# Kernel tuning notes

Hardware: AMD Instinct MI355X
Metric: run time of the kernel (lower is better)

Reference implementation:

```python
import jax, jax.numpy as jnp
import numpy as np

B, T, D = 4, 2048, 2048
DV = 1024
T_IMG, N_LAT = 8, 64
H, DH = 16, 64
INNER = H * DH
EPS = 1e-5


def setup_inputs() -> dict:
    key = jax.random.key(0)
    ks = jax.random.split(key, 8)
    x = jax.random.normal(ks[0], (B, T, D), dtype=jnp.float32)
    media = jax.random.normal(ks[1], (B, T_IMG, N_LAT, DV), dtype=jnp.float32)
    # exactly T_IMG media tokens per sequence, evenly spaced
    pos = (jnp.arange(T_IMG) + 1) * (T // (T_IMG + 1))
    media_locations = jnp.zeros((B, T), dtype=bool).at[:, pos].set(True)
    gamma = jnp.ones((D,), dtype=jnp.float32)
    beta = jnp.zeros((D,), dtype=jnp.float32)
    Wq = jax.random.normal(ks[2], (D, INNER), dtype=jnp.float32) * (D ** -0.5)
    Wkv = jax.random.normal(ks[3], (DV, 2 * INNER), dtype=jnp.float32) * (DV ** -0.5)
    Wout = jax.random.normal(ks[4], (INNER, D), dtype=jnp.float32) * (INNER ** -0.5)
    return {"x": x, "media": media, "media_locations": media_locations,
            "gamma": gamma, "beta": beta, "Wq": Wq, "Wkv": Wkv, "Wout": Wout}


def reference(x, media, media_locations, gamma, beta, Wq, Wkv, Wout):
    scale = DH ** -0.5
    # LayerNorm
    mu = jnp.mean(x, axis=-1, keepdims=True)
    var = jnp.mean(jnp.square(x - mu), axis=-1, keepdims=True)
    xn = (x - mu) * jax.lax.rsqrt(var + EPS) * gamma + beta
    q = xn @ Wq                                   # (B,T,INNER)
    media_f = media.reshape(B, T_IMG * N_LAT, DV)  # (B,J,DV)
    kv = media_f @ Wkv                             # (B,J,2*INNER)
    k, v = jnp.split(kv, 2, axis=-1)
    q = q.reshape(B, T, H, DH).transpose(0, 2, 1, 3) * scale   # (B,H,T,DH)
    k = k.reshape(B, -1, H, DH).transpose(0, 2, 1, 3)          # (B,H,J,DH)
    v = v.reshape(B, -1, H, DH).transpose(0, 2, 1, 3)
    sim = jnp.einsum('bhid,bhjd->bhij', q, k)      # (B,H,T,J)
    # media-location mask: text attends only to its immediately preceding media
    text_time = jnp.cumsum(media_locations.astype(jnp.int32), axis=-1)  # (B,T)
    media_time = jnp.arange(T_IMG, dtype=jnp.int32) + 1                 # (J_img,)
    media_time = jnp.repeat(media_time, N_LAT)                          # (J,)
    mask = text_time[:, None, :, None] == media_time[None, None, None, :]  # (B,1,T,J)
    neg = -jnp.finfo(sim.dtype).max
    sim = jnp.where(mask, sim, neg)
    sim = sim - jax.lax.stop_gradient(jnp.max(sim, axis=-1, keepdims=True))
    attn = jax.nn.softmax(sim, axis=-1)
    # zero attention for text positions with no preceding media
    no_media = (text_time == 0)[:, None, :, None]  # (B,1,T,1)
    attn = jnp.where(no_media, 0.0, attn)
    out = jnp.einsum('bhij,bhjd->bhid', attn, v)   # (B,H,T,DH)
    out = out.transpose(0, 2, 1, 3).reshape(B, T, INNER)
    return out @ Wout
```

## Files before the change

kernel.cpp:

```cpp
#include <hip/hip_runtime.h>
#include <hip/hip_bf16.h>

#define B_ 4
#define T_ 2048
#define D_ 2048
#define DV_ 1024
#define TIMG_ 8
#define NLAT_ 64
#define H_ 16
#define DH_ 64
#define INNER_ 1024
#define J_ (TIMG_ * NLAT_)

using f32x4 = __attribute__((ext_vector_type(4))) float;
using bf16x8 = __attribute__((ext_vector_type(8))) short;
using bf16x4 = __attribute__((ext_vector_type(4))) short;

__device__ __forceinline__ unsigned short f2bf(float f) {
  union { float f; unsigned int u; } c{f};
  unsigned int r = c.u + 0x7FFFu + ((c.u >> 16) & 1u);
  return (unsigned short)(r >> 16);
}

__device__ __forceinline__ void stage16(const unsigned short* g, unsigned short* l) {
  __builtin_amdgcn_global_load_lds(
      (const __attribute__((address_space(1))) unsigned int*)g,
      (__attribute__((address_space(3))) unsigned int*)l, 16, 0, 0);
}

__global__ __launch_bounds__(256) void prep_kernel(
    const float* __restrict__ x, const void* __restrict__ locs,
    const float* __restrict__ g, const float* __restrict__ bta,
    const float* __restrict__ Wq, const float* __restrict__ Wkv,
    const float* __restrict__ Wout, const float* __restrict__ media,
    unsigned short* __restrict__ xn, int* __restrict__ img_idx,
    unsigned short* __restrict__ wqt, unsigned short* __restrict__ wkvt,
    unsigned short* __restrict__ woutt, unsigned short* __restrict__ medb) {
  __shared__ __align__(16) float smf[64 * 68];
  const int tid = threadIdx.x;
  int blk = blockIdx.x;

  if (blk < 2048) {
    const int lane = tid & 63;
    const int row = blk * 4 + (tid >> 6);
    const float4* xr = (const float4*)(x + (size_t)row * D_);
    float4 v[8];
#pragma unroll
    for (int i = 0; i < 8; ++i) v[i] = xr[i * 64 + lane];
    float s = 0.f, sq = 0.f;
#pragma unroll
    for (int i = 0; i < 8; ++i) {
      s += v[i].x + v[i].y + v[i].z + v[i].w;
      sq += v[i].x * v[i].x + v[i].y * v[i].y + v[i].z * v[i].z + v[i].w * v[i].w;
    }
#pragma unroll
    for (int off = 32; off > 0; off >>= 1) {
      s += __shfl_xor(s, off);
      sq += __shfl_xor(sq, off);
    }
    const float mu = s * (1.0f / D_);
    const float rstd = rsqrtf(sq * (1.0f / D_) - mu * mu + 1e-5f);
    const float4* gv4 = (const float4*)g;
    const float4* bv4 = (const float4*)bta;
    ushort4* o4 = (ushort4*)(xn + (size_t)row * D_);
#pragma unroll
    for (int i = 0; i < 8; ++i) {
      float4 gv = gv4[i * 64 + lane];
      float4 bv = bv4[i * 64 + lane];
      o4[i * 64 + lane] = make_ushort4(f2bf((v[i].x - mu) * rstd * gv.x + bv.x),
                                       f2bf((v[i].y - mu) * rstd * gv.y + bv.y),
                                       f2bf((v[i].z - mu) * rstd * gv.z + bv.z),
                                       f2bf((v[i].w - mu) * rstd * gv.w + bv.w));
    }
    return;
  }
  blk -= 2048;
  if (blk < 4) {
    int* sm = (int*)smf;
    const int b = blk;
    const unsigned char* u8 = (const unsigned char*)locs;
    int cnt = 0;
    for (int i = tid; i < B_ * T_; i += 256) cnt += (u8[i] != 0) ? 1 : 0;
    sm[tid] = cnt;
    __syncthreads();
    for (int off = 128; off > 0; off >>= 1) {
      if (tid < off) sm[tid] += sm[tid + off];
      __syncthreads();
    }
    const bool u8mode = (sm[0] == B_ * TIMG_);
    __syncthreads();
    const int base = b * T_ + tid * 8;
    const int* i32 = (const int*)locs;
    int v[8];
    int ts = 0;
#pragma unroll
    for (int j = 0; j < 8; ++j) {
      v[j] = u8mode ? (u8[base + j] != 0 ? 1 : 0) : (i32[base + j] != 0 ? 1 : 0);
      ts += v[j];
    }
    sm[tid] = ts;
    __syncthreads();
    for (int off = 1; off < 256; off <<= 1) {
      int add = (tid >= off) ? sm[tid - off] : 0;
      __syncthreads();
      sm[tid] += add;
      __syncthreads();
    }
    int acc = sm[tid] - ts;
#pragma unroll
    for (int j = 0; j < 8; ++j) {
      acc += v[j];
      img_idx[base + j] = acc - 1;
    }
    return;
  }
  blk -= 4;
  if (blk < 1536) {
    const float* tin;
    unsigned short* tout;
    int R, C, bx, by;
    float scale = 1.0f;
    if (blk < 512) {
      tin = Wq; tout = wqt; R = D_; C = INNER_; by = blk >> 4; bx = blk & 15; scale = 0.125f;
    } else if (blk < 1024) {
      blk -= 512;
      tin = Wkv; tout = wkvt; R = DV_; C = 2 * INNER_; by = blk >> 5; bx = blk & 31;
    } else {
      blk -= 1024;
      tin = Wout; tout = woutt; R = INNER_; C = D_; by = blk >> 5; bx = blk & 31;
    }
    const int br = by * 64, bc = bx * 64;
    float (*tile)[68] = (float(*)[68])smf;
    const int r = tid >> 4;
    const int c4 = (tid & 15) * 4;
#pragma unroll
    for (int rr = 0; rr < 4; ++rr)
      *(float4*)&tile[r + rr * 16][c4] =
          *(const float4*)&tin[(size_t)(br + r + rr * 16) * C + bc + c4];
    __syncthreads();
    const int oc = tid >> 2;
    const int rb = (tid & 3) * 16;
    bf16x8 o0, o1;
#pragma unroll
    for (int e = 0; e < 8; ++e) {
      o0[e] = (short)f2bf(tile[rb + e][oc] * scale);
      o1[e] = (short)f2bf(tile[rb + 8 + e][oc] * scale);
    }
    unsigned short* op = tout + (size_t)(bc + oc) * R + br + rb;
    *(bf16x8*)op = o0;
    *(bf16x8*)(op + 8) = o1;
    return;
  }
  blk -= 1536;
  const int i = blk * 512 + tid * 2;
  float4 a = ((const float4*)media)[i];
  float4 b2 = ((const float4*)media)[i + 1];
  ((ushort4*)medb)[i] = make_ushort4(f2bf(a.x), f2bf(a.y), f2bf(a.z), f2bf(a.w));
  ((ushort4*)medb)[i + 1] = make_ushort4(f2bf(b2.x), f2bf(b2.y), f2bf(b2.z), f2bf(b2.w));
}

__global__ void vtrans(const unsigned short* __restrict__ kvb, unsigned short* __restrict__ vt) {
  __shared__ unsigned short tile[32][33];
  const int jt = blockIdx.x * 32;
  const int dt = blockIdx.y * 32;
  const int b = blockIdx.z;
  const int tx = threadIdx.x, ty = threadIdx.y;
#pragma unroll
  for (int i = ty; i < 32; i += 8)
    tile[i][tx] = kvb[(size_t)(b * J_ + jt + i) * (2 * INNER_) + INNER_ + dt + tx];
  __syncthreads();
#pragma unroll
  for (int i = ty; i < 32; i += 8)
    vt[(size_t)(b * INNER_ + dt + i) * J_ + jt + tx] = tile[tx][i];
}

template <bool BF16OUT>
__global__ __launch_bounds__(512, 2) void gemm_bt2(const unsigned short* __restrict__ Ag,
                                                   const unsigned short* __restrict__ Bg,
                                                   void* __restrict__ Cv,
                                                   int M, int N, int K) {
  __shared__ __align__(16) unsigned short lds[65536];
  const int tid = threadIdx.x;
  const int lane = tid & 63;
  const int wave = tid >> 6;
  const int l15 = lane & 15;
  const int lg8 = (lane >> 4) << 3;
  const int wr64 = (wave >> 2) << 6;
  const int wc16 = (wave & 3) << 4;

  const int nwg = gridDim.x;
  int wg = ((int)blockIdx.x & 7) * (nwg >> 3) + ((int)blockIdx.x >> 3);
  const int gridM = M >> 7;
  const long row0 = (long)(wg % gridM) << 7;
  const long col0 = (long)(wg / gridM) << 8;

  auto stA = [&](int t, int r) {
    const int i = r * 512 + tid;
    const int row = i >> 3;
    const int c = (i & 7) ^ (row & 7);
    stage16(Ag + (size_t)(row0 + row) * K + (t << 6) + c * 8,
            &lds[(t & 1) * 8192 + i * 8]);
  };
  auto stB = [&](int t, int r) {
    const int i = r * 512 + tid;
    const int row = i >> 3;
    const int c = (i & 7) ^ (row & 7);
    stage16(Bg + (size_t)(col0 + row) * K + (t << 6) + c * 8,
            &lds[16384 + (t % 3) * 16384 + i * 8]);
  };

  const int NT = K >> 6;
  stB(0, 0); stB(0, 1); stB(0, 2); stB(0, 3);
  stA(0, 0); stA(0, 1);
  stB(1, 0); stB(1, 1); stB(1, 2); stB(1, 3);
  asm volatile("s_waitcnt vmcnt(4)" ::: "memory");
  asm volatile("s_barrier" ::: "memory");

  f32x4 acc[4][4] = {};
  for (int t = 0; t < NT; ++t) {
    const unsigned short* Ab = &lds[(t & 1) * 8192];
    const unsigned short* Bb = &lds[16384 + (t % 3) * 16384];
    bf16x8 af[4][2], bfr[4][2];
#pragma unroll
    for (int m = 0; m < 4; ++m)
#pragma unroll
      for (int kk = 0; kk < 2; ++kk) {
        const int row = wr64 + m * 16 + l15;
        af[m][kk] = *(const bf16x8*)(Ab + row * 64 + ((kk * 32 + lg8) ^ ((row & 7) << 3)));
      }
#pragma unroll
    for (int n = 0; n < 2; ++n)
#pragma unroll
      for (int kk = 0; kk < 2; ++kk) {
        const int brow = n * 64 + wc16 + l15;
        bfr[n][kk] = *(const bf16x8*)(Bb + brow * 64 + ((kk * 32 + lg8) ^ ((brow & 7) << 3)));
      }
    if (t + 1 < NT) { stA(t + 1, 0); stA(t + 1, 1); }
    if (t + 2 < NT) { stB(t + 2, 0); stB(t + 2, 1); }
    asm volatile("s_barrier" ::: "memory");
    asm volatile("s_waitcnt lgkmcnt(0)" ::: "memory");
    __builtin_amdgcn_s_setprio(1);
#pragma unroll
    for (int m = 0; m < 4; ++m)
#pragma unroll
      for (int n = 0; n < 2; ++n)
#pragma unroll
        for (int kk = 0; kk < 2; ++kk)
          acc[m][n] = __builtin_amdgcn_mfma_f32_16x16x32_bf16(af[m][kk], bfr[n][kk], acc[m][n], 0, 0, 0);
    __builtin_amdgcn_s_setprio(0);
    asm volatile("s_barrier" ::: "memory");
#pragma unroll
    for (int n = 2; n < 4; ++n)
#pragma unroll
      for (int kk = 0; kk < 2; ++kk) {
        const int brow = n * 64 + wc16 + l15;
        bfr[n][kk] = *(const bf16x8*)(Bb + brow * 64 + ((kk * 32 + lg8) ^ ((brow & 7) << 3)));
      }
    if (t + 2 < NT) {
      stB(t + 2, 2); stB(t + 2, 3);
      asm volatile("s_waitcnt vmcnt(4)" ::: "memory");
    } else {
      asm volatile("s_waitcnt vmcnt(0)" ::: "memory");
    }
    asm volatile("s_barrier" ::: "memory");
    asm volatile("s_waitcnt lgkmcnt(0)" ::: "memory");
    __builtin_amdgcn_s_setprio(1);
#pragma unroll
    for (int m = 0; m < 4; ++m)
#pragma unroll
      for (int n = 2; n < 4; ++n)
#pragma unroll
        for (int kk = 0; kk < 2; ++kk)
          acc[m][n] = __builtin_amdgcn_mfma_f32_16x16x32_bf16(af[m][kk], bfr[n][kk], acc[m][n], 0, 0, 0);
    __builtin_amdgcn_s_setprio(0);
    asm volatile("s_barrier" ::: "memory");
  }

  const int cr = (lane >> 4) << 2;
#pragma unroll
  for (int m = 0; m < 4; ++m)
#pragma unroll
    for (int n = 0; n < 4; ++n)
#pragma unroll
      for (int j = 0; j < 4; ++j) {
        const size_t idx = (row0 + wr64 + m * 16 + cr + j) * (size_t)N + col0 + n * 64 + wc16 + l15;
        if constexpr (BF16OUT)
          ((unsigned short*)Cv)[idx] = f2bf(acc[m][n][j]);
        else
          ((float*)Cv)[idx] = acc[m][n][j];
      }
}

template <bool BF16OUT>
__global__ __launch_bounds__(512, 2) void gemm256(const unsigned short* __restrict__ Ag,
                                                  const unsigned short* __restrict__ Bg,
                                                  void* __restrict__ Cv,
                                                  int M, int N, int K) {
  __shared__ __align__(16) unsigned short lds[2][32768];
  const int tid = threadIdx.x;
  const int lane = tid & 63;
  const int wave = tid >> 6;
  const int l15 = lane & 15;
  const int lg8 = (lane >> 4) << 3;
  const int wm = (wave >> 2) << 7;
  const int wn = (wave & 3) << 6;

  const int nwg = gridDim.x;
  int wg = ((int)blockIdx.x & 7) * (nwg >> 3) + ((int)blockIdx.x >> 3);
  const int gridM = M >> 8;
  const long row0 = (long)(wg % gridM) << 8;
  const long col0 = (long)(wg / gridM) << 8;

  auto stA = [&](int buf, int kt, int r) {
    const int i = r * 512 + tid;
    const int row = i >> 3;
    const int c = (i & 7) ^ (row & 7);
    stage16(Ag + (size_t)(row0 + row) * K + kt + c * 8, &lds[buf][i * 8]);
  };
  auto stB = [&](int buf, int kt, int r) {
    const int i = r * 512 + tid;
    const int row = i >> 3;
    const int c = (i & 7) ^ (row & 7);
    stage16(Bg + (size_t)(col0 + row) * K + kt + c * 8, &lds[buf][16384 + i * 8]);
  };

  const int NT = K >> 6;
  stB(0, 0, 0); stB(0, 0, 1); stB(0, 0, 2); stB(0, 0, 3);
  stA(0, 0, 0); stA(0, 0, 1); stA(0, 0, 2); stA(0, 0, 3);
  stB(1, 64, 0); stB(1, 64, 1); stB(1, 64, 2); stB(1, 64, 3);
  asm volatile("s_waitcnt vmcnt(4)" ::: "memory");
  asm volatile("s_barrier" ::: "memory");

  f32x4 acc[8][4] = {};
  int cur = 0;
  for (int t = 0; t < NT; ++t, cur ^= 1) {
    const unsigned short* Ab = &lds[cur][0];
    const unsigned short* Bb = &lds[cur][16384];
    bf16x8 af[4][2], bfr[4][2];
    const int ktn = (t + 1) << 6;
    const int ktn2 = (t + 2) << 6;
#pragma unroll
    for (int m = 0; m < 4; ++m)
#pragma unroll
      for (int kk = 0; kk < 2; ++kk) {
        const int row = wm + m * 16 + l15;
        af[m][kk] = *(const bf16x8*)(Ab + row * 64 + ((kk * 32 + lg8) ^ ((row & 7) << 3)));
      }
#pragma unroll
    for (int n = 0; n < 2; ++n)
#pragma unroll
      for (int kk = 0; kk < 2; ++kk) {
        const int brow = wn + n * 16 + l15;
        bfr[n][kk] = *(const bf16x8*)(Bb + brow * 64 + ((kk * 32 + lg8) ^ ((brow & 7) << 3)));
      }
    if (t + 1 < NT) { stA(cur ^ 1, ktn, 0); stA(cur ^ 1, ktn, 1); }
    asm volatile("s_barrier" ::: "memory");
    asm volatile("s_waitcnt lgkmcnt(0)" ::: "memory");
    __builtin_amdgcn_s_setprio(1);
#pragma unroll
    for (int m = 0; m < 4; ++m)
#pragma unroll
      for (int n = 0; n < 2; ++n)
#pragma unroll
        for (int kk = 0; kk < 2; ++kk)
          acc[m][n] = __builtin_amdgcn_mfma_f32_16x16x32_bf16(af[m][kk], bfr[n][kk], acc[m][n], 0, 0, 0);
    __builtin_amdgcn_s_setprio(0);
    asm volatile("s_barrier" ::: "memory");
#pragma unroll
    for (int n = 2; n < 4; ++n)
#pragma unroll
      for (int kk = 0; kk < 2; ++kk) {
        const int brow = wn + n * 16 + l15;
        bfr[n][kk] = *(const bf16x8*)(Bb + brow * 64 + ((kk * 32 + lg8) ^ ((brow & 7) << 3)));
      }
    if (t + 1 < NT) { stA(cur ^ 1, ktn, 2); stA(cur ^ 1, ktn, 3); }
    asm volatile("s_barrier" ::: "memory");
    asm volatile("s_waitcnt lgkmcnt(0)" ::: "memory");
    __builtin_amdgcn_s_setprio(1);
#pragma unroll
    for (int m = 0; m < 4; ++m)
#pragma unroll
      for (int n = 2; n < 4; ++n)
#pragma unroll
        for (int kk = 0; kk < 2; ++kk)
          acc[m][n] = __builtin_amdgcn_mfma_f32_16x16x32_bf16(af[m][kk], bfr[n][kk], acc[m][n], 0, 0, 0);
    __builtin_amdgcn_s_setprio(0);
    asm volatile("s_barrier" ::: "memory");
#pragma unroll
    for (int m = 0; m < 4; ++m)
#pragma unroll
      for (int kk = 0; kk < 2; ++kk) {
        const int row = wm + (m + 4) * 16 + l15;
        af[m][kk] = *(const bf16x8*)(Ab + row * 64 + ((kk * 32 + lg8) ^ ((row & 7) << 3)));
      }
    if (t + 2 < NT) { stB(cur, ktn2, 0); stB(cur, ktn2, 1); }
    asm volatile("s_barrier" ::: "memory");
    asm volatile("s_waitcnt lgkmcnt(0)" ::: "memory");
    __builtin_amdgcn_s_setprio(1);
#pragma unroll
    for (int m = 0; m < 4; ++m)
#pragma unroll
      for (int n = 0; n < 2; ++n)
#pragma unroll
        for (int kk = 0; kk < 2; ++kk)
          acc[m + 4][n] = __builtin_amdgcn_mfma_f32_16x16x32_bf16(af[m][kk], bfr[n][kk], acc[m + 4][n], 0, 0, 0);
    __builtin_amdgcn_s_setprio(0);
    asm volatile("s_barrier" ::: "memory");
    if (t + 2 < NT) { stB(cur, ktn2, 2); stB(cur, ktn2, 3); }
    asm volatile("s_waitcnt vmcnt(4)" ::: "memory");
    asm volatile("s_barrier" ::: "memory");
    __builtin_amdgcn_s_setprio(1);
#pragma unroll
    for (int m = 0; m < 4; ++m)
#pragma unroll
      for (int n = 2; n < 4; ++n)
#pragma unroll
        for (int kk = 0; kk < 2; ++kk)
          acc[m + 4][n] = __builtin_amdgcn_mfma_f32_16x16x32_bf16(af[m][kk], bfr[n][kk], acc[m + 4][n], 0, 0, 0);
    __builtin_amdgcn_s_setprio(0);
    asm volatile("s_barrier" ::: "memory");
  }

  const int cr = (lane >> 4) << 2;
#pragma unroll
  for (int m = 0; m < 8; ++m)
#pragma unroll
    for (int n = 0; n < 4; ++n)
#pragma unroll
      for (int j = 0; j < 4; ++j) {
        const size_t idx = (row0 + wm + m * 16 + cr + j) * (size_t)N + col0 + wn + n * 16 + l15;
        if constexpr (BF16OUT)
          ((unsigned short*)Cv)[idx] = f2bf(acc[m][n][j]);
        else
          ((float*)Cv)[idx] = acc[m][n][j];
      }
}

__global__ __launch_bounds__(256) void attn2_kernel(
    const unsigned short* __restrict__ qb,
    const unsigned short* __restrict__ kvb,
    const unsigned short* __restrict__ vt,
    const int* __restrict__ img_idx,
    unsigned short* __restrict__ attn_out) {
  __shared__ unsigned short Pl[4][64 * 72];
  const int tid = threadIdx.x;
  const int lane = tid & 63;
  const int w = tid >> 6;
  int bid = blockIdx.x;
  const int hg = bid & 3; bid >>= 2;
  const int tile = bid & 31; bid >>= 5;
  const int b = bid;
  const int t0 = tile * 64;
  const int h = hg * 4 + w;
  const int l15 = lane & 15;
  const int lg = lane >> 4;

  const int* ii = img_idx + b * T_ + t0;
  int myimg = ii[lane];
  int tmin = myimg, tmax = myimg;
#pragma unroll
  for (int off = 1; off < 64; off <<= 1) {
    tmin = min(tmin, __shfl_xor(tmin, off));
    tmax = max(tmax, __shfl_xor(tmax, off));
  }
  unsigned short* op = attn_out + (size_t)(b * T_ + t0) * INNER_ + h * DH_;
  if (tmin < 0) {
    for (int r = 0; r < 64; ++r)
      if (ii[r] < 0) op[(size_t)r * INNER_ + lane] = 0;
  }
  if (tmax < 0) return;

  bf16x8 qa[4][2];
  const unsigned short* qrow = qb + (size_t)(b * T_ + t0) * INNER_ + h * DH_;
#pragma unroll
  for (int m = 0; m < 4; ++m)
#pragma unroll
    for (int kk = 0; kk < 2; ++kk)
      qa[m][kk] = *(const bf16x8*)(qrow + (size_t)(l15 + m * 16) * INNER_ + kk * 32 + lg * 8);

  unsigned short* pw = Pl[w];
  for (int img = max(tmin, 0); img <= tmax; ++img) {
    const unsigned short* Kb = kvb + (size_t)(b * J_ + img * NLAT_) * (2 * INNER_) + h * DH_;
    f32x4 acc[4][4] = {};
#pragma unroll
    for (int kk = 0; kk < 2; ++kk) {
      bf16x8 bfr[4];
#pragma unroll
      for (int n = 0; n < 4; ++n)
        bfr[n] = *(const bf16x8*)(Kb + (size_t)(l15 + n * 16) * (2 * INNER_) + kk * 32 + lg * 8);
#pragma unroll
      for (int m = 0; m < 4; ++m)
#pragma unroll
        for (int n = 0; n < 4; ++n)
          acc[m][n] = __builtin_amdgcn_mfma_f32_16x16x32_bf16(qa[m][kk], bfr[n], acc[m][n], 0, 0, 0);
    }
#pragma unroll
    for (int m = 0; m < 4; ++m) {
#pragma unroll
      for (int j = 0; j < 4; ++j) {
        float mx = fmaxf(fmaxf(acc[m][0][j], acc[m][1][j]), fmaxf(acc[m][2][j], acc[m][3][j]));
#pragma unroll
        for (int off = 1; off < 16; off <<= 1) mx = fmaxf(mx, __shfl_xor(mx, off));
        float sum = 0.f;
#pragma unroll
        for (int n = 0; n < 4; ++n) {
          float e = __expf(acc[m][n][j] - mx);
          acc[m][n][j] = e;
          sum += e;
        }
#pragma unroll
        for (int off = 1; off < 16; off <<= 1) sum += __shfl_xor(sum, off);
        const float ri = 1.0f / sum;
        const int row = m * 16 + lg * 4 + j;
#pragma unroll
        for (int n = 0; n < 4; ++n)
          pw[row * 72 + n * 16 + l15] = f2bf(acc[m][n][j] * ri);
      }
    }
    const unsigned short* Vb = vt + (size_t)(b * INNER_ + h * DH_) * J_ + img * NLAT_;
    f32x4 oacc[4][4] = {};
#pragma unroll
    for (int kk = 0; kk < 2; ++kk) {
      bf16x8 pa[4], bfr[4];
#pragma unroll
      for (int m = 0; m < 4; ++m) {
        bf16x4 lo = *(const bf16x4*)(pw + (m * 16 + l15) * 72 + kk * 32 + lg * 8);
        bf16x4 hi = *(const bf16x4*)(pw + (m * 16 + l15) * 72 + kk * 32 + lg * 8 + 4);
        bf16x8 v;
#pragma unroll
        for (int e = 0; e < 4; ++e) { v[e] = lo[e]; v[e + 4] = hi[e]; }
        pa[m] = v;
      }
#pragma unroll
      for (int n = 0; n < 4; ++n)
        bfr[n] = *(const bf16x8*)(Vb + (size_t)(l15 + n * 16) * J_ + kk * 32 + lg * 8);
#pragma unroll
      for (int m = 0; m < 4; ++m)
#pragma unroll
        for (int n = 0; n < 4; ++n)
          oacc[m][n] = __builtin_amdgcn_mfma_f32_16x16x32_bf16(pa[m], bfr[n], oacc[m][n], 0, 0, 0);
    }
#pragma unroll
    for (int m = 0; m < 4; ++m)
#pragma unroll
      for (int j = 0; j < 4; ++j) {
        const int row = m * 16 + lg * 4 + j;
        if (ii[row] == img) {
#pragma unroll
          for (int n = 0; n < 4; ++n)
            op[(size_t)row * INNER_ + n * 16 + l15] = f2bf(oacc[m][n][j]);
        }
      }
  }
}

extern "C" void kernel_launch(void* const* d_in, const int* in_sizes, int n_in,
                              void* d_out, int out_size, void* d_ws, size_t ws_size,
                              hipStream_t stream) {
  const float* x = (const float*)d_in[0];
  const float* media = (const float*)d_in[1];
  const void* mloc = d_in[2];
  const float* gamma = (const float*)d_in[3];
  const float* beta = (const float*)d_in[4];
  const float* Wq = (const float*)d_in[5];
  const float* Wkv = (const float*)d_in[6];
  const float* Wout = (const float*)d_in[7];
  float* out = (float*)d_out;

  char* ws = (char*)d_ws;
  unsigned short* xn = (unsigned short*)(ws);
  unsigned short* wqt = (unsigned short*)(ws + 33554432);
  unsigned short* wkvt = (unsigned short*)(ws + 37748736);
  unsigned short* woutt = (unsigned short*)(ws + 41943040);
  unsigned short* medb = (unsigned short*)(ws + 46137344);
  unsigned short* qb = (unsigned short*)(ws + 50331648);
  unsigned short* kvb = (unsigned short*)(ws + 67108864);
  unsigned short* vt = (unsigned short*)(ws + 75497472);
  int* img_idx = (int*)(ws + 79691776);
  unsigned short* attn_out = xn;

  prep_kernel<<<4612, 256, 0, stream>>>(x, mloc, gamma, beta, Wq, Wkv, Wout, media,
                                        xn, img_idx, wqt, wkvt, woutt, medb);
  gemm_bt2<true><<<(B_ * T_ / 128) * (INNER_ / 256), 512, 0, stream>>>(xn, wqt, qb, B_ * T_, INNER_, D_);
  gemm_bt2<true><<<(B_ * J_ / 128) * (2 * INNER_ / 256), 512, 0, stream>>>(medb, wkvt, kvb, B_ * J_, 2 * INNER_, DV_);
  vtrans<<<dim3(J_ / 32, INNER_ / 32, B_), dim3(32, 8), 0, stream>>>(kvb, vt);
  attn2_kernel<<<B_ * (T_ / 64) * 4, 256, 0, stream>>>(qb, kvb, vt, img_idx, attn_out);
  gemm256<false><<<(B_ * T_ / 256) * (D_ / 256), 512, 0, stream>>>(attn_out, woutt, out, B_ * T_, D_, INNER_);
}
```

Measured before the change: 156.7 us.

## Split prep kernel and fuse remaining prep work into the Q-projection GEMM launch

```diff
diff --git a/kernel.cpp b/kernel.cpp
--- a/kernel.cpp
+++ b/kernel.cpp
@@ -28,14 +28,10 @@
       (__attribute__((address_space(3))) unsigned int*)l, 16, 0, 0);
 }
 
-__global__ __launch_bounds__(256) void prep_kernel(
-    const float* __restrict__ x, const void* __restrict__ locs,
-    const float* __restrict__ g, const float* __restrict__ bta,
-    const float* __restrict__ Wq, const float* __restrict__ Wkv,
-    const float* __restrict__ Wout, const float* __restrict__ media,
-    unsigned short* __restrict__ xn, int* __restrict__ img_idx,
-    unsigned short* __restrict__ wqt, unsigned short* __restrict__ wkvt,
-    unsigned short* __restrict__ woutt, unsigned short* __restrict__ medb) {
+__global__ __launch_bounds__(256) void prepA_kernel(
+    const float* __restrict__ x, const float* __restrict__ g,
+    const float* __restrict__ bta, const float* __restrict__ Wq,
+    unsigned short* __restrict__ xn, unsigned short* __restrict__ wqt) {
   __shared__ __align__(16) float smf[64 * 68];
   const int tid = threadIdx.x;
   int blk = blockIdx.x;
@@ -75,9 +71,138 @@
     return;
   }
   blk -= 2048;
-  if (blk < 4) {
-    int* sm = (int*)smf;
-    const int b = blk;
+  const int by = blk >> 4, bx = blk & 15;
+  const int br = by * 64, bc = bx * 64;
+  float (*tile)[68] = (float(*)[68])smf;
+  const int r = tid >> 4;
+  const int c4 = (tid & 15) * 4;
+#pragma unroll
+  for (int rr = 0; rr < 4; ++rr)
+    *(float4*)&tile[r + rr * 16][c4] =
+        *(const float4*)&Wq[(size_t)(br + r + rr * 16) * INNER_ + bc + c4];
+  __syncthreads();
+  const int oc = tid >> 2;
+  const int rb = (tid & 3) * 16;
+  bf16x8 o0, o1;
+#pragma unroll
+  for (int e = 0; e < 8; ++e) {
+    o0[e] = (short)f2bf(tile[rb + e][oc] * 0.125f);
+    o1[e] = (short)f2bf(tile[rb + 8 + e][oc] * 0.125f);
+  }
+  unsigned short* op = wqt + (size_t)(bc + oc) * D_ + br + rb;
+  *(bf16x8*)op = o0;
+  *(bf16x8*)(op + 8) = o1;
+}
+
+template <bool BF16OUT>
+__device__ __forceinline__ void gemm128_body(int wg, unsigned char* smem,
+                                             const unsigned short* Ag,
+                                             const unsigned short* Bg,
+                                             void* Cv, int M, int N, int K) {
+  unsigned short* lds = (unsigned short*)smem;
+  const int tid = threadIdx.x;
+  const int lane = tid & 63;
+  const int wave = tid >> 6;
+  const int l15 = lane & 15;
+  const int kg = lane >> 4;
+  const int wm = (wave >> 1) << 6;
+  const int wn = (wave & 1) << 6;
+  const int gridM = M >> 7;
+  const long row0 = (long)(wg % gridM) << 7;
+  const long col0 = (long)(wg / gridM) << 7;
+
+  auto stT = [&](const unsigned short* G, long base0, int t, int r, int bufoff) {
+    const int j = r * 256 + tid;
+    const int rp = j >> 3;
+    const int u = (j & 7) ^ (rp & 7);
+    const int row = (rp << 1) | (u >> 2);
+    const int k8 = (u & 3) << 3;
+    stage16(G + (base0 + row) * K + (t << 5) + k8, &lds[bufoff + j * 8]);
+  };
+
+  const int NT = K >> 5;
+  stT(Bg, col0, 0, 0, 8192); stT(Bg, col0, 0, 1, 8192);
+  stT(Ag, row0, 0, 0, 0);    stT(Ag, row0, 0, 1, 0);
+  stT(Bg, col0, 1, 0, 8192 + 4096); stT(Bg, col0, 1, 1, 8192 + 4096);
+  asm volatile("s_waitcnt vmcnt(2)" ::: "memory");
+  asm volatile("s_barrier" ::: "memory");
+
+  f32x4 acc[4][4] = {};
+  for (int t = 0; t < NT; ++t) {
+    const unsigned short* Ab = &lds[(t & 1) * 4096];
+    const unsigned short* Bb = &lds[8192 + (t % 3) * 4096];
+    bf16x8 af[4], bfr[4];
+#pragma unroll
+    for (int m = 0; m < 4; ++m) {
+      const int r = wm + m * 16 + l15;
+      const int rp = r >> 1;
+      const int s = (((r & 1) << 2) | kg) ^ (rp & 7);
+      af[m] = *(const bf16x8*)(Ab + rp * 64 + s * 8);
+    }
+#pragma unroll
+    for (int n = 0; n < 4; ++n) {
+      const int r = wn + n * 16 + l15;
+      const int rp = r >> 1;
+      const int s = (((r & 1) << 2) | kg) ^ (rp & 7);
+      bfr[n] = *(const bf16x8*)(Bb + rp * 64 + s * 8);
+    }
+    if (t + 1 < NT) {
+      stT(Ag, row0, t + 1, 0, ((t + 1) & 1) * 4096);
+      stT(Ag, row0, t + 1, 1, ((t + 1) & 1) * 4096);
+    }
+    if (t + 2 < NT) {
+      stT(Bg, col0, t + 2, 0, 8192 + ((t + 2) % 3) * 4096);
+      stT(Bg, col0, t + 2, 1, 8192 + ((t + 2) % 3) * 4096);
+    }
+    asm volatile("s_waitcnt lgkmcnt(0)" ::: "memory");
+    __builtin_amdgcn_s_setprio(1);
+#pragma unroll
+    for (int m = 0; m < 4; ++m)
+#pragma unroll
+      for (int n = 0; n < 4; ++n)
+        acc[m][n] = __builtin_amdgcn_mfma_f32_16x16x32_bf16(af[m], bfr[n], acc[m][n], 0, 0, 0);
+    __builtin_amdgcn_s_setprio(0);
+    if (t + 2 < NT)
+      asm volatile("s_waitcnt vmcnt(2)" ::: "memory");
+    else
+      asm volatile("s_waitcnt vmcnt(0)" ::: "memory");
+    asm volatile("s_barrier" ::: "memory");
+  }
+
+  const int cr = (lane >> 4) << 2;
+#pragma unroll
+  for (int m = 0; m < 4; ++m)
+#pragma unroll
+    for (int n = 0; n < 4; ++n)
+#pragma unroll
+      for (int j = 0; j < 4; ++j) {
+        const size_t idx = (row0 + wm + m * 16 + cr + j) * (size_t)N + col0 + wn + n * 16 + l15;
+        if constexpr (BF16OUT)
+          ((unsigned short*)Cv)[idx] = f2bf(acc[m][n][j]);
+        else
+          ((float*)Cv)[idx] = acc[m][n][j];
+      }
+}
+
+__global__ __launch_bounds__(256, 4) void g1_fused(
+    const unsigned short* __restrict__ xn, const unsigned short* __restrict__ wqt,
+    unsigned short* __restrict__ qb,
+    const void* __restrict__ locs, const float* __restrict__ Wkv,
+    const float* __restrict__ Wout, const float* __restrict__ media,
+    int* __restrict__ img_idx, unsigned short* __restrict__ wkvt,
+    unsigned short* __restrict__ woutt, unsigned short* __restrict__ medb) {
+  __shared__ __align__(16) unsigned char smem[40960];
+  const int tid = threadIdx.x;
+  const int bid = blockIdx.x;
+  const bool isg = (bid < 2560) && (bid % 5 == 0);
+  if (isg) {
+    gemm128_body<true>(bid / 5, smem, xn, wqt, qb, B_ * T_, INNER_, D_);
+    return;
+  }
+  int pid = (bid < 2560) ? bid - bid / 5 - 1 : bid - 512;
+  if (pid < 4) {
+    int* sm = (int*)smem;
+    const int b = pid;
     const unsigned char* u8 = (const unsigned char*)locs;
     int cnt = 0;
     for (int i = tid; i < B_ * T_; i += 256) cnt += (u8[i] != 0) ? 1 : 0;
@@ -114,45 +239,36 @@
     }
     return;
   }
-  blk -= 4;
-  if (blk < 1536) {
-    const float* tin;
-    unsigned short* tout;
-    int R, C, bx, by;
-    float scale = 1.0f;
-    if (blk < 512) {
-      tin = Wq; tout = wqt; R = D_; C = INNER_; by = blk >> 4; bx = blk & 15; scale = 0.125f;
-    } else if (blk < 1024) {
-      blk -= 512;
-      tin = Wkv; tout = wkvt; R = DV_; C = 2 * INNER_; by = blk >> 5; bx = blk & 31;
-    } else {
-      blk -= 1024;
-      tin = Wout; tout = woutt; R = INNER_; C = D_; by = blk >> 5; bx = blk & 31;
-    }
+  pid -= 4;
+  if (pid < 1024) {
+    const float* tin = (pid < 512) ? Wkv : Wout;
+    unsigned short* tout = (pid < 512) ? wkvt : woutt;
+    int blk = pid & 511;
+    const int by = blk >> 5, bx = blk & 31;
     const int br = by * 64, bc = bx * 64;
-    float (*tile)[68] = (float(*)[68])smf;
+    float (*tile)[68] = (float(*)[68])smem;
     const int r = tid >> 4;
     const int c4 = (tid & 15) * 4;
 #pragma unroll
     for (int rr = 0; rr < 4; ++rr)
       *(float4*)&tile[r + rr * 16][c4] =
-          *(const float4*)&tin[(size_t)(br + r + rr * 16) * C + bc + c4];
+          *(const float4*)&tin[(size_t)(br + r + rr * 16) * (2 * INNER_) + bc + c4];
     __syncthreads();
     const int oc = tid >> 2;
     const int rb = (tid & 3) * 16;
     bf16x8 o0, o1;
 #pragma unroll
     for (int e = 0; e < 8; ++e) {
-      o0[e] = (short)f2bf(tile[rb + e][oc] * scale);
-      o1[e] = (short)f2bf(tile[rb + 8 + e][oc] * scale);
-    }
-    unsigned short* op = tout + (size_t)(bc + oc) * R + br + rb;
+      o0[e] = (short)f2bf(tile[rb + e][oc]);
+      o1[e] = (short)f2bf(tile[rb + 8 + e][oc]);
+    }
+    unsigned short* op = tout + (size_t)(bc + oc) * DV_ + br + rb;
     *(bf16x8*)op = o0;
     *(bf16x8*)(op + 8) = o1;
     return;
   }
-  blk -= 1536;
-  const int i = blk * 512 + tid * 2;
+  pid -= 1024;
+  const int i = pid * 512 + tid * 2;
   float4 a = ((const float4*)media)[i];
   float4 b2 = ((const float4*)media)[i + 1];
   ((ushort4*)medb)[i] = make_ushort4(f2bf(a.x), f2bf(a.y), f2bf(a.z), f2bf(a.w));
@@ -579,9 +695,9 @@
   int* img_idx = (int*)(ws + 79691776);
   unsigned short* attn_out = xn;
 
-  prep_kernel<<<4612, 256, 0, stream>>>(x, mloc, gamma, beta, Wq, Wkv, Wout, media,
-                                        xn, img_idx, wqt, wkvt, woutt, medb);
-  gemm_bt2<true><<<(B_ * T_ / 128) * (INNER_ / 256), 512, 0, stream>>>(xn, wqt, qb, B_ * T_, INNER_, D_);
+  prepA_kernel<<<2560, 256, 0, stream>>>(x, gamma, beta, Wq, xn, wqt);
+  g1_fused<<<2564, 256, 0, stream>>>(xn, wqt, qb, mloc, Wkv, Wout, media,
+                                     img_idx, wkvt, woutt, medb);
   gemm_bt2<true><<<(B_ * J_ / 128) * (2 * INNER_ / 256), 512, 0, stream>>>(medb, wkvt, kvb, B_ * J_, 2 * INNER_, DV_);
   vtrans<<<dim3(J_ / 32, INNER_ / 32, B_), dim3(32, 8), 0, stream>>>(kvb, vt);
   attn2_kernel<<<B_ * (T_ / 64) * 4, 256, 0, stream>>>(qb, kvb, vt, img_idx, attn_out);
```

Result: slower. 178.0 us (+13.6%).

## Fold LayerNorm into Q projection GEMM via gamma-scaled weights and epilogue correction

Applied to the files above, without the earlier changes.

```diff
diff --git a/kernel.cpp b/kernel.cpp
--- a/kernel.cpp
+++ b/kernel.cpp
@@ -29,52 +29,38 @@
 }
 
 __global__ __launch_bounds__(256) void prep_kernel(
-    const float* __restrict__ x, const void* __restrict__ locs,
+    const void* __restrict__ locs,
     const float* __restrict__ g, const float* __restrict__ bta,
     const float* __restrict__ Wq, const float* __restrict__ Wkv,
     const float* __restrict__ Wout, const float* __restrict__ media,
-    unsigned short* __restrict__ xn, int* __restrict__ img_idx,
+    int* __restrict__ img_idx,
     unsigned short* __restrict__ wqt, unsigned short* __restrict__ wkvt,
-    unsigned short* __restrict__ woutt, unsigned short* __restrict__ medb) {
+    unsigned short* __restrict__ woutt, unsigned short* __restrict__ medb,
+    float* __restrict__ uvec, float* __restrict__ vvec) {
   __shared__ __align__(16) float smf[64 * 68];
   const int tid = threadIdx.x;
   int blk = blockIdx.x;
 
-  if (blk < 2048) {
-    const int lane = tid & 63;
-    const int row = blk * 4 + (tid >> 6);
-    const float4* xr = (const float4*)(x + (size_t)row * D_);
-    float4 v[8];
-#pragma unroll
-    for (int i = 0; i < 8; ++i) v[i] = xr[i * 64 + lane];
-    float s = 0.f, sq = 0.f;
-#pragma unroll
-    for (int i = 0; i < 8; ++i) {
-      s += v[i].x + v[i].y + v[i].z + v[i].w;
-      sq += v[i].x * v[i].x + v[i].y * v[i].y + v[i].z * v[i].z + v[i].w * v[i].w;
-    }
-#pragma unroll
-    for (int off = 32; off > 0; off >>= 1) {
-      s += __shfl_xor(s, off);
-      sq += __shfl_xor(sq, off);
-    }
-    const float mu = s * (1.0f / D_);
-    const float rstd = rsqrtf(sq * (1.0f / D_) - mu * mu + 1e-5f);
-    const float4* gv4 = (const float4*)g;
-    const float4* bv4 = (const float4*)bta;
-    ushort4* o4 = (ushort4*)(xn + (size_t)row * D_);
-#pragma unroll
-    for (int i = 0; i < 8; ++i) {
-      float4 gv = gv4[i * 64 + lane];
-      float4 bv = bv4[i * 64 + lane];
-      o4[i * 64 + lane] = make_ushort4(f2bf((v[i].x - mu) * rstd * gv.x + bv.x),
-                                       f2bf((v[i].y - mu) * rstd * gv.y + bv.y),
-                                       f2bf((v[i].z - mu) * rstd * gv.z + bv.z),
-                                       f2bf((v[i].w - mu) * rstd * gv.w + bv.w));
+  if (blk < 16) {
+    const int col = blk * 64 + (tid & 63);
+    const int kc = tid >> 6;
+    float su = 0.f, sv = 0.f;
+    for (int k = kc * 512; k < kc * 512 + 512; ++k) {
+      const float w = Wq[(size_t)k * INNER_ + col];
+      su += g[k] * w;
+      sv += bta[k] * w;
+    }
+    float* s1 = smf;
+    float* s2 = smf + 256;
+    s1[tid] = su; s2[tid] = sv;
+    __syncthreads();
+    if (tid < 64) {
+      uvec[blk * 64 + tid] = 0.125f * (s1[tid] + s1[tid + 64] + s1[tid + 128] + s1[tid + 192]);
+      vvec[blk * 64 + tid] = 0.125f * (s2[tid] + s2[tid + 64] + s2[tid + 128] + s2[tid + 192]);
     }
     return;
   }
-  blk -= 2048;
+  blk -= 16;
   if (blk < 4) {
     int* sm = (int*)smf;
     const int b = blk;
@@ -115,20 +101,8 @@
     return;
   }
   blk -= 4;
-  if (blk < 1536) {
-    const float* tin;
-    unsigned short* tout;
-    int R, C, bx, by;
-    float scale = 1.0f;
-    if (blk < 512) {
-      tin = Wq; tout = wqt; R = D_; C = INNER_; by = blk >> 4; bx = blk & 15; scale = 0.125f;
-    } else if (blk < 1024) {
-      blk -= 512;
-      tin = Wkv; tout = wkvt; R = DV_; C = 2 * INNER_; by = blk >> 5; bx = blk & 31;
-    } else {
-      blk -= 1024;
-      tin = Wout; tout = woutt; R = INNER_; C = D_; by = blk >> 5; bx = blk & 31;
-    }
+  if (blk < 512) {
+    const int by = blk >> 4, bx = blk & 15;
     const int br = by * 64, bc = bx * 64;
     float (*tile)[68] = (float(*)[68])smf;
     const int r = tid >> 4;
@@ -136,27 +110,190 @@
 #pragma unroll
     for (int rr = 0; rr < 4; ++rr)
       *(float4*)&tile[r + rr * 16][c4] =
-          *(const float4*)&tin[(size_t)(br + r + rr * 16) * C + bc + c4];
+          *(const float4*)&Wq[(size_t)(br + r + rr * 16) * INNER_ + bc + c4];
     __syncthreads();
     const int oc = tid >> 2;
     const int rb = (tid & 3) * 16;
     bf16x8 o0, o1;
 #pragma unroll
     for (int e = 0; e < 8; ++e) {
-      o0[e] = (short)f2bf(tile[rb + e][oc] * scale);
-      o1[e] = (short)f2bf(tile[rb + 8 + e][oc] * scale);
-    }
-    unsigned short* op = tout + (size_t)(bc + oc) * R + br + rb;
+      o0[e] = (short)f2bf(tile[rb + e][oc] * g[br + rb + e] * 0.125f);
+      o1[e] = (short)f2bf(tile[rb + 8 + e][oc] * g[br + rb + 8 + e] * 0.125f);
+    }
+    unsigned short* op = wqt + (size_t)(bc + oc) * D_ + br + rb;
     *(bf16x8*)op = o0;
     *(bf16x8*)(op + 8) = o1;
     return;
   }
-  blk -= 1536;
+  blk -= 512;
+  if (blk < 1024) {
+    const float* tin = (blk < 512) ? Wkv : Wout;
+    unsigned short* tout = (blk < 512) ? wkvt : woutt;
+    int idx = blk & 511;
+    const int by = idx >> 5, bx = idx & 31;
+    const int br = by * 64, bc = bx * 64;
+    float (*tile)[68] = (float(*)[68])smf;
+    const int r = tid >> 4;
+    const int c4 = (tid & 15) * 4;
+#pragma unroll
+    for (int rr = 0; rr < 4; ++rr)
+      *(float4*)&tile[r + rr * 16][c4] =
+          *(const float4*)&tin[(size_t)(br + r + rr * 16) * (2 * INNER_) + bc + c4];
+    __syncthreads();
+    const int oc = tid >> 2;
+    const int rb = (tid & 3) * 16;
+    bf16x8 o0, o1;
+#pragma unroll
+    for (int e = 0; e < 8; ++e) {
+      o0[e] = (short)f2bf(tile[rb + e][oc]);
+      o1[e] = (short)f2bf(tile[rb + 8 + e][oc]);
+    }
+    unsigned short* op = tout + (size_t)(bc + oc) * DV_ + br + rb;
+    *(bf16x8*)op = o0;
+    *(bf16x8*)(op + 8) = o1;
+    return;
+  }
+  blk -= 1024;
   const int i = blk * 512 + tid * 2;
   float4 a = ((const float4*)media)[i];
   float4 b2 = ((const float4*)media)[i + 1];
   ((ushort4*)medb)[i] = make_ushort4(f2bf(a.x), f2bf(a.y), f2bf(a.z), f2bf(a.w));
   ((ushort4*)medb)[i + 1] = make_ushort4(f2bf(b2.x), f2bf(b2.y), f2bf(b2.z), f2bf(b2.w));
+}
+
+__global__ __launch_bounds__(512, 2) void gemm1_ln(
+    const float* __restrict__ Xg, const unsigned short* __restrict__ Bg,
+    unsigned short* __restrict__ Cv,
+    const float* __restrict__ uvec, const float* __restrict__ vvec) {
+  const int M = B_ * T_, N = INNER_, K = D_;
+  __shared__ __align__(16) unsigned short lds[65536];
+  const int tid = threadIdx.x;
+  const int lane = tid & 63;
+  const int wave = tid >> 6;
+  const int l15 = lane & 15;
+  const int lg8 = (lane >> 4) << 3;
+  const int wr64 = (wave >> 2) << 6;
+  const int wc16 = (wave & 3) << 4;
+
+  const int nwg = gridDim.x;
+  int wg = ((int)blockIdx.x & 7) * (nwg >> 3) + ((int)blockIdx.x >> 3);
+  const int gridM = M >> 7;
+  const long row0 = (long)(wg % gridM) << 7;
+  const long col0 = (long)(wg / gridM) << 8;
+
+  const int ar = tid >> 2;
+  const int aq = tid & 3;
+  const float4* xrow = (const float4*)(Xg + (size_t)(row0 + ar) * K) + aq * 4;
+
+  auto stB = [&](int t, int r) {
+    const int i = r * 512 + tid;
+    const int row = i >> 3;
+    const int c = (i & 7) ^ (row & 7);
+    stage16(Bg + (size_t)(col0 + row) * K + (t << 6) + c * 8,
+            &lds[16384 + (t % 3) * 16384 + i * 8]);
+  };
+
+  float s_part = 0.f, sq_part = 0.f;
+  float4 a0, a1, a2, a3;
+  auto aload = [&](int t) {
+    const float4* p = xrow + t * 16;
+    a0 = p[0]; a1 = p[1]; a2 = p[2]; a3 = p[3];
+  };
+  auto acvt = [&](int t) {
+    unsigned short* Ab = &lds[(t & 1) * 8192];
+    float v0[8] = {a0.x, a0.y, a0.z, a0.w, a1.x, a1.y, a1.z, a1.w};
+    float v1[8] = {a2.x, a2.y, a2.z, a2.w, a3.x, a3.y, a3.z, a3.w};
+    bf16x8 w0, w1;
+#pragma unroll
+    for (int e = 0; e < 8; ++e) {
+      s_part += v0[e] + v1[e];
+      sq_part += v0[e] * v0[e] + v1[e] * v1[e];
+      w0[e] = (short)f2bf(v0[e]);
+      w1[e] = (short)f2bf(v1[e]);
+    }
+    *(bf16x8*)(Ab + ar * 64 + (((aq * 2) ^ (ar & 7)) << 3)) = w0;
+    *(bf16x8*)(Ab + ar * 64 + (((aq * 2 + 1) ^ (ar & 7)) << 3)) = w1;
+  };
+
+  const int NT = K >> 6;
+  aload(0); acvt(0);
+  aload(1);
+  stB(0, 0); stB(0, 1); stB(0, 2); stB(0, 3);
+  stB(1, 0); stB(1, 1); stB(1, 2); stB(1, 3);
+  asm volatile("s_waitcnt vmcnt(4)" ::: "memory");
+  asm volatile("s_waitcnt lgkmcnt(0)" ::: "memory");
+  asm volatile("s_barrier" ::: "memory");
+
+  f32x4 acc[4][4] = {};
+  for (int t = 0; t < NT; ++t) {
+    const unsigned short* Ab = &lds[(t & 1) * 8192];
+    const unsigned short* Bb = &lds[16384 + (t % 3) * 16384];
+    bf16x8 af[4][2], bfr[4][2];
+#pragma unroll
+    for (int m = 0; m < 4; ++m)
+#pragma unroll
+      for (int kk = 0; kk < 2; ++kk) {
+        const int row = wr64 + m * 16 + l15;
+        af[m][kk] = *(const bf16x8*)(Ab + row * 64 + ((kk * 32 + lg8) ^ ((row & 7) << 3)));
+      }
+#pragma unroll
+    for (int n = 0; n < 4; ++n)
+#pragma unroll
+      for (int kk = 0; kk < 2; ++kk) {
+        const int brow = n * 64 + wc16 + l15;
+        bfr[n][kk] = *(const bf16x8*)(Bb + brow * 64 + ((kk * 32 + lg8) ^ ((brow & 7) << 3)));
+      }
+    if (t + 1 < NT) {
+      acvt(t + 1);
+      if (t + 2 < NT) aload(t + 2);
+    }
+    if (t + 2 < NT) { stB(t + 2, 0); stB(t + 2, 1); stB(t + 2, 2); stB(t + 2, 3); }
+    asm volatile("s_waitcnt lgkmcnt(0)" ::: "memory");
+    __builtin_amdgcn_s_setprio(1);
+#pragma unroll
+    for (int m = 0; m < 4; ++m)
+#pragma unroll
+      for (int n = 0; n < 4; ++n)
+#pragma unroll
+        for (int kk = 0; kk < 2; ++kk)
+          acc[m][n] = __builtin_amdgcn_mfma_f32_16x16x32_bf16(af[m][kk], bfr[n][kk], acc[m][n], 0, 0, 0);
+    __builtin_amdgcn_s_setprio(0);
+    if (t + 2 < NT)
+      asm volatile("s_waitcnt vmcnt(8)" ::: "memory");
+    else
+      asm volatile("s_waitcnt vmcnt(0)" ::: "memory");
+    asm volatile("s_barrier" ::: "memory");
+  }
+
+  float* sred = (float*)lds;
+  sred[tid] = s_part;
+  sred[512 + tid] = sq_part;
+  __syncthreads();
+  if (tid < 128) {
+    float s = sred[tid * 4] + sred[tid * 4 + 1] + sred[tid * 4 + 2] + sred[tid * 4 + 3];
+    float sq = sred[512 + tid * 4] + sred[512 + tid * 4 + 1] + sred[512 + tid * 4 + 2] + sred[512 + tid * 4 + 3];
+    float mu = s * (1.0f / D_);
+    sred[1024 + tid] = mu;
+    sred[1152 + tid] = rsqrtf(sq * (1.0f / D_) - mu * mu + 1e-5f);
+  }
+  __syncthreads();
+
+  const int cr = (lane >> 4) << 2;
+#pragma unroll
+  for (int n = 0; n < 4; ++n) {
+    const long col = col0 + n * 64 + wc16 + l15;
+    const float uu = uvec[col];
+    const float vv = vvec[col];
+#pragma unroll
+    for (int m = 0; m < 4; ++m)
+#pragma unroll
+      for (int j = 0; j < 4; ++j) {
+        const int lr = wr64 + m * 16 + cr + j;
+        const float mu = sred[1024 + lr];
+        const float rstd = sred[1152 + lr];
+        Cv[(row0 + lr) * (size_t)N + col] = f2bf(rstd * (acc[m][n][j] - mu * uu) + vv);
+      }
+  }
 }
 
 __global__ void vtrans(const unsigned short* __restrict__ kvb, unsigned short* __restrict__ vt) {
@@ -568,7 +705,7 @@
   float* out = (float*)d_out;
 
   char* ws = (char*)d_ws;
-  unsigned short* xn = (unsigned short*)(ws);
+  unsigned short* attn_out = (unsigned short*)(ws);
   unsigned short* wqt = (unsigned short*)(ws + 33554432);
   unsigned short* wkvt = (unsigned short*)(ws + 37748736);
   unsigned short* woutt = (unsigned short*)(ws + 41943040);
@@ -577,11 +714,12 @@
   unsigned short* kvb = (unsigned short*)(ws + 67108864);
   unsigned short* vt = (unsigned short*)(ws + 75497472);
   int* img_idx = (int*)(ws + 79691776);
-  unsigned short* attn_out = xn;
-
-  prep_kernel<<<4612, 256, 0, stream>>>(x, mloc, gamma, beta, Wq, Wkv, Wout, media,
-                                        xn, img_idx, wqt, wkvt, woutt, medb);
-  gemm_bt2<true><<<(B_ * T_ / 128) * (INNER_ / 256), 512, 0, stream>>>(xn, wqt, qb, B_ * T_, INNER_, D_);
+  float* uvec = (float*)(ws + 79724544);
+  float* vvec = (float*)(ws + 79728640);
+
+  prep_kernel<<<2580, 256, 0, stream>>>(mloc, gamma, beta, Wq, Wkv, Wout, media,
+                                        img_idx, wqt, wkvt, woutt, medb, uvec, vvec);
+  gemm1_ln<<<256, 512, 0, stream>>>(x, wqt, qb, uvec, vvec);
   gemm_bt2<true><<<(B_ * J_ / 128) * (2 * INNER_ / 256), 512, 0, stream>>>(medb, wkvt, kvb, B_ * J_, 2 * INNER_, DV_);
   vtrans<<<dim3(J_ / 32, INNER_ / 32, B_), dim3(32, 8), 0, stream>>>(kvb, vt);
   attn2_kernel<<<B_ * (T_ / 64) * 4, 256, 0, stream>>>(qb, kvb, vt, img_idx, attn_out);
```

Measured after the change: 271.5 us. 73.3% more time.
